# Kernel tuning notes

Measured on AMD Instinct MI355X. Metric: run time of the kernel, lower is better.

Reference implementation:

```python
import jax, jax.numpy as jnp
import numpy as np

N, D, H, E, K = 4096, 512, 2048, 8, 2  # tokens, input_size, hidden_size, num_experts, top_k


def setup_inputs() -> dict:
    key = jax.random.key(0)
    ks = jax.random.split(key, 4)
    x = jax.random.normal(ks[0], (N, D), dtype=jnp.float32)
    # torch init: weights ~ N(0, 0.001), biases zero
    Wg = jax.random.normal(ks[1], (D, E), dtype=jnp.float32) * 0.001
    bg = jnp.zeros((E,), jnp.float32)
    W1 = jax.random.normal(ks[2], (E, D, H), dtype=jnp.float32) * 0.001
    b1 = jnp.zeros((E, H), jnp.float32)
    W2 = jax.random.normal(ks[3], (E, H, D), dtype=jnp.float32) * 0.001
    b2 = jnp.zeros((E, D), jnp.float32)
    return {"x": x, "Wg": Wg, "bg": bg, "W1": W1, "b1": b1, "W2": W2, "b2": b2}


def reference(x, Wg, bg, W1, b1, W2, b2):
    # Gating: softmax over experts
    gates = jax.nn.softmax(x @ Wg + bg, axis=-1)            # [N, E]
    top_w, top_i = jax.lax.top_k(gates, K)                  # [N, K]
    top_w = top_w / jnp.sum(top_w, axis=-1, keepdims=True)  # renormalize

    # Expert MLP (fc1 -> fc2, no nonlinearity per source). Vectorized across all
    # experts, then gather the top-k selected outputs per token.
    h1 = jnp.einsum('nd,edh->neh', x, W1) + b1              # [N, E, H]
    all_out = jnp.einsum('neh,ehd->ned', h1, W2) + b2       # [N, E, D]
    sel = jnp.take_along_axis(all_out, top_i[:, :, None], axis=1)  # [N, K, D]

    combined = jnp.einsum('nkd,nk->nd', sel, top_w)         # [N, D]

    # usage counts: scatter-add of (detached) top-k weights per expert
    usage = jnp.zeros((E,), x.dtype).at[top_i.reshape(-1)].add(
        jax.lax.stop_gradient(top_w).reshape(-1))
    return combined, usage
```

## Files before the change

kernel.cpp:

```cpp
#include <hip/hip_runtime.h>
#include <hip/hip_bf16.h>


#define N_TOK 4096
#define DIM   512
#define HID   2048
#define NEXP  8
#define TOTSLOT (2 * N_TOK)
#define M1TILE 72
#define M2TILE 144

typedef __attribute__((ext_vector_type(8))) short short8;
typedef __attribute__((ext_vector_type(4))) float f32x4;

static __device__ __forceinline__ unsigned short f2bf(float f) {
    __hip_bfloat16 b = __float2bfloat16(f);
    return *reinterpret_cast<unsigned short*>(&b);
}
static __device__ __forceinline__ float bf2f(unsigned short u) {
    return __uint_as_float((unsigned)u << 16);
}

static __device__ __forceinline__ void load16_to_lds(const void* g, void* l) {
    __builtin_amdgcn_global_load_lds(
        (const __attribute__((address_space(1))) unsigned int*)g,
        (__attribute__((address_space(3))) unsigned int*)l, 16, 0, 0);
}

__global__ __launch_bounds__(256) void gating_kernel(
    const float* __restrict__ x, const float* __restrict__ Wg,
    const float* __restrict__ bg,
    int* __restrict__ cnt, int* __restrict__ te, float* __restrict__ tw,
    float* __restrict__ usage, unsigned short* __restrict__ Xb)
{
    __shared__ int   lcnt[NEXP];
    __shared__ float lus[NEXP];
    int tid = threadIdx.x;
    if (tid < NEXP) { lcnt[tid] = 0; lus[tid] = 0.f; }
    __syncthreads();

    int wave = tid >> 6;
    int lane = tid & 63;

    for (int t = 0; t < 4; ++t) {
        int n = blockIdx.x * 16 + wave * 4 + t;

        float acc[NEXP];
#pragma unroll
        for (int e = 0; e < NEXP; ++e) acc[e] = 0.f;

#pragma unroll
        for (int it = 0; it < DIM / 64; ++it) {
            int d = it * 64 + lane;
            float xv = x[n * DIM + d];
            Xb[n * DIM + d] = f2bf(xv);
            float4 wa = *(const float4*)&Wg[d * NEXP];
            float4 wb = *(const float4*)&Wg[d * NEXP + 4];
            acc[0] += xv * wa.x; acc[1] += xv * wa.y;
            acc[2] += xv * wa.z; acc[3] += xv * wa.w;
            acc[4] += xv * wb.x; acc[5] += xv * wb.y;
            acc[6] += xv * wb.z; acc[7] += xv * wb.w;
        }
#pragma unroll
        for (int m = 32; m >= 1; m >>= 1) {
#pragma unroll
            for (int e = 0; e < NEXP; ++e)
                acc[e] += __shfl_xor(acc[e], m, 64);
        }
        if (lane == 0) {
            float l[NEXP];
#pragma unroll
            for (int e = 0; e < NEXP; ++e) l[e] = acc[e] + bg[e];
            int i0 = 0;
#pragma unroll
            for (int e = 1; e < NEXP; ++e) if (l[e] > l[i0]) i0 = e;
            int i1 = (i0 == 0) ? 1 : 0;
#pragma unroll
            for (int e = 0; e < NEXP; ++e)
                if (e != i0 && l[e] > l[i1]) i1 = e;
            float w0 = 1.f / (1.f + expf(l[i1] - l[i0]));
            float w1 = 1.f - w0;
            te[n * 2] = i0; te[n * 2 + 1] = i1;
            tw[n * 2] = w0; tw[n * 2 + 1] = w1;
            atomicAdd(&lcnt[i0], 1);
            atomicAdd(&lcnt[i1], 1);
            atomicAdd(&lus[i0], w0);
            atomicAdd(&lus[i1], w1);
        }
    }
    __syncthreads();
    if (tid < NEXP) {
        if (lcnt[tid]) atomicAdd(&cnt[tid], lcnt[tid]);
        if (lus[tid] != 0.f) atomicAdd(&usage[tid], lus[tid]);
    }
}

__global__ void prefix_kernel(const int* __restrict__ cnt,
                              int* __restrict__ offs, int* __restrict__ fill,
                              int* __restrict__ tb128, int* __restrict__ tb64,
                              int* __restrict__ ntile)
{
    if (threadIdx.x == 0) {
        int s = 0, a = 0, b = 0;
        for (int e = 0; e < NEXP; ++e) {
            offs[e] = s; s += cnt[e];
            tb128[e] = a; a += (cnt[e] + 127) >> 7;
            tb64[e]  = b; b += (cnt[e] + 63) >> 6;
        }
        tb128[NEXP] = a; tb64[NEXP] = b;
        ntile[0] = a; ntile[1] = b;
    }
    if (threadIdx.x < NEXP) fill[threadIdx.x] = 0;
}

__global__ __launch_bounds__(256) void scatter_kernel(
    int* __restrict__ te, const float* __restrict__ tw,
    const int* __restrict__ offs, int* __restrict__ fill,
    int* __restrict__ btok, float* __restrict__ bwt)
{
    __shared__ int lcnt[NEXP];
    __shared__ int gbase[NEXP];
    int tid = threadIdx.x;
    if (tid < NEXP) lcnt[tid] = 0;
    __syncthreads();
    int n = blockIdx.x * 256 + tid;
    int e0 = te[n * 2], e1 = te[n * 2 + 1];
    int l0 = atomicAdd(&lcnt[e0], 1);
    int l1 = atomicAdd(&lcnt[e1], 1);
    __syncthreads();
    if (tid < NEXP) gbase[tid] = atomicAdd(&fill[tid], lcnt[tid]);
    __syncthreads();
    int s0 = offs[e0] + gbase[e0] + l0;
    int s1 = offs[e1] + gbase[e1] + l1;
    btok[s0] = n; bwt[s0] = tw[n * 2];
    btok[s1] = n; bwt[s1] = tw[n * 2 + 1];
    te[n * 2] = s0; te[n * 2 + 1] = s1;
}

__global__ __launch_bounds__(256) void transpose_cvt_kernel(
    const float* __restrict__ in, unsigned short* __restrict__ out,
    int R, int C)
{
    __shared__ unsigned short tile[64][65];
    int e = blockIdx.z;
    const float* src = in + (size_t)e * R * C;
    unsigned short* dst = out + (size_t)e * R * C;
    int r0 = blockIdx.x * 64, c0 = blockIdx.y * 64;
    int tid = threadIdx.x;
    int rr = tid >> 2, cb = (tid & 3) * 16;
#pragma unroll
    for (int i = 0; i < 4; ++i) {
        float4 v = *(const float4*)&src[(size_t)(r0 + rr) * C + c0 + cb + i * 4];
        tile[rr][cb + i * 4 + 0] = f2bf(v.x);
        tile[rr][cb + i * 4 + 1] = f2bf(v.y);
        tile[rr][cb + i * 4 + 2] = f2bf(v.z);
        tile[rr][cb + i * 4 + 3] = f2bf(v.w);
    }
    __syncthreads();
#pragma unroll
    for (int i = 0; i < 4; ++i) {
        ushort4 u;
        u.x = tile[cb + i * 4 + 0][rr];
        u.y = tile[cb + i * 4 + 1][rr];
        u.z = tile[cb + i * 4 + 2][rr];
        u.w = tile[cb + i * 4 + 3][rr];
        *(ushort4*)&dst[(size_t)(c0 + rr) * R + r0 + cb + i * 4] = u;
    }
}


__global__ __launch_bounds__(256) void gemm1_kernel(
    const unsigned short* __restrict__ Xb, const unsigned short* __restrict__ W1t,
    const float* __restrict__ b1, const int* __restrict__ cnt,
    const int* __restrict__ offs, const int* __restrict__ btok,
    const int* __restrict__ tb128, const int* __restrict__ ntile,
    unsigned short* __restrict__ H1)
{
    __shared__ __align__(16) unsigned short Ws[128 * 64];
    __shared__ __align__(16) unsigned short Xs[128 * 64];
    __shared__ int tok_s[128];

    int bx = blockIdx.x;
    int ti = (bx & 7) * (M1TILE / 8) + (bx >> 3);
    if (ti >= ntile[0]) return;
    int e = 0;
#pragma unroll
    for (int k = 1; k < NEXP; ++k) if (ti >= tb128[k]) e = k;
    int tt = ti - tb128[e];
    int ht = blockIdx.y;
    int cn = cnt[e];
    int off_e = offs[e];
    int tid = threadIdx.x;

    if (tid < 128) {
        int lr = tt * 128 + tid;
        tok_s[tid] = (lr < cn) ? btok[off_e + lr] : 0;
    }
    __syncthreads();

    int wave = tid >> 6, lane = tid & 63;
    int mbase = (wave >> 1) * 64, nbase = (wave & 1) * 64;
    int quad = lane >> 4, lcol = lane & 15;
    f32x4 acc[4][4];
#pragma unroll
    for (int mi = 0; mi < 4; ++mi)
#pragma unroll
        for (int ni = 0; ni < 4; ++ni)
            acc[mi][ni] = (f32x4){0.f, 0.f, 0.f, 0.f};

    int Rb = tid >> 3, pc = tid & 7;
    const unsigned short* Wsrc = W1t + ((size_t)e * HID + ht * 128) * DIM;

    for (int k0 = 0; k0 < DIM; k0 += 64) {
#pragma unroll
        for (int p = 0; p < 4; ++p) {
            int R = Rb + p * 32;
            int c = pc ^ (R & 7);
            load16_to_lds(&Wsrc[(size_t)R * DIM + k0 + c * 8], &Ws[R * 64 + pc * 8]);
            load16_to_lds(&Xb[(size_t)tok_s[R] * DIM + k0 + c * 8], &Xs[R * 64 + pc * 8]);
        }
        __syncthreads();
#pragma unroll
        for (int h = 0; h < 2; ++h) {
            int cs = ((h * 4 + quad) ^ (lcol & 7)) * 8;
            short8 a[4], b[4];
#pragma unroll
            for (int i = 0; i < 4; ++i) {
                a[i] = *(const short8*)&Ws[(mbase + i * 16 + lcol) * 64 + cs];
                b[i] = *(const short8*)&Xs[(nbase + i * 16 + lcol) * 64 + cs];
            }
#pragma unroll
            for (int mi = 0; mi < 4; ++mi)
#pragma unroll
                for (int ni = 0; ni < 4; ++ni)
                    acc[mi][ni] = __builtin_amdgcn_mfma_f32_16x16x32_bf16(
                        a[mi], b[ni], acc[mi][ni], 0, 0, 0);
        }
        __syncthreads();
    }

    float4 bv[4];
#pragma unroll
    for (int mi = 0; mi < 4; ++mi)
        bv[mi] = *(const float4*)&b1[e * HID + ht * 128 + mbase + mi * 16 + quad * 4];
#pragma unroll
    for (int ni = 0; ni < 4; ++ni) {
        int tn = tt * 128 + nbase + ni * 16 + lcol;
        if (tn >= cn) continue;
        size_t srow = (size_t)(off_e + tn) * HID + ht * 128;
#pragma unroll
        for (int mi = 0; mi < 4; ++mi) {
            int hh = mbase + mi * 16 + quad * 4;
            ushort4 u;
            u.x = f2bf(acc[mi][ni][0] + bv[mi].x);
            u.y = f2bf(acc[mi][ni][1] + bv[mi].y);
            u.z = f2bf(acc[mi][ni][2] + bv[mi].z);
            u.w = f2bf(acc[mi][ni][3] + bv[mi].w);
            *(ushort4*)&H1[srow + hh] = u;
        }
    }
}

#define KSPLIT 2
#define KCH (HID / KSPLIT)

__global__ __launch_bounds__(256) void gemm2_kernel(
    const unsigned short* __restrict__ H1, const unsigned short* __restrict__ W2t,
    const float* __restrict__ b2, const int* __restrict__ cnt,
    const int* __restrict__ offs, const float* __restrict__ bwt,
    const int* __restrict__ tb64, const int* __restrict__ ntile,
    unsigned short* __restrict__ O)
{
    __shared__ __align__(16) unsigned short Ws[128 * 64];
    __shared__ __align__(16) unsigned short Hs[64 * 64];
    __shared__ float wt_s[64];

    int bx = blockIdx.x;
    int ti = (bx & 7) * (M2TILE / 8) + (bx >> 3);
    if (ti >= ntile[1]) return;
    int e = 0;
#pragma unroll
    for (int k = 1; k < NEXP; ++k) if (ti >= tb64[k]) e = k;
    int tt = ti - tb64[e];
    int dt = blockIdx.y, kz = blockIdx.z;
    int cn = cnt[e];
    int off_e = offs[e];
    int sb = off_e + tt * 64;
    int tid = threadIdx.x;

    if (tid < 64) {
        int lr = tt * 64 + tid;
        wt_s[tid] = (lr < cn) ? bwt[off_e + lr] : 0.f;
    }

    int wave = tid >> 6, lane = tid & 63;
    int nbase = wave * 32;
    int quad = lane >> 4, lcol = lane & 15;
    f32x4 acc[4][2];
#pragma unroll
    for (int mi = 0; mi < 4; ++mi)
#pragma unroll
        for (int ni = 0; ni < 2; ++ni)
            acc[mi][ni] = (f32x4){0.f, 0.f, 0.f, 0.f};

    int Rb = tid >> 3, pc = tid & 7;
    const unsigned short* Wsrc = W2t + ((size_t)e * DIM + dt * 128) * HID;

    for (int k0 = kz * KCH; k0 < (kz + 1) * KCH; k0 += 64) {
#pragma unroll
        for (int p = 0; p < 4; ++p) {
            int R = Rb + p * 32;
            int c = pc ^ (R & 7);
            load16_to_lds(&Wsrc[(size_t)R * HID + k0 + c * 8], &Ws[R * 64 + pc * 8]);
        }
#pragma unroll
        for (int p = 0; p < 2; ++p) {
            int R = Rb + p * 32;
            int c = pc ^ (R & 7);
            int sr = sb + R; if (sr > TOTSLOT - 1) sr = TOTSLOT - 1;
            load16_to_lds(&H1[(size_t)sr * HID + k0 + c * 8], &Hs[R * 64 + pc * 8]);
        }
        __syncthreads();
#pragma unroll
        for (int h = 0; h < 2; ++h) {
            int cs = ((h * 4 + quad) ^ (lcol & 7)) * 8;
            short8 a[4], b[2];
#pragma unroll
            for (int i = 0; i < 4; ++i)
                a[i] = *(const short8*)&Hs[(i * 16 + lcol) * 64 + cs];
#pragma unroll
            for (int i = 0; i < 2; ++i)
                b[i] = *(const short8*)&Ws[(nbase + i * 16 + lcol) * 64 + cs];
#pragma unroll
            for (int mi = 0; mi < 4; ++mi)
#pragma unroll
                for (int ni = 0; ni < 2; ++ni)
                    acc[mi][ni] = __builtin_amdgcn_mfma_f32_16x16x32_bf16(
                        a[mi], b[ni], acc[mi][ni], 0, 0, 0);
        }
        __syncthreads();
    }

    unsigned short* Oe = O + ((size_t)kz * TOTSLOT + sb) * DIM + dt * 128;
#pragma unroll
    for (int ni = 0; ni < 2; ++ni) {
        int dl = nbase + ni * 16 + lcol;
        float bv = (kz == 0) ? b2[e * DIM + dt * 128 + dl] : 0.f;
#pragma unroll
        for (int mi = 0; mi < 4; ++mi) {
            int rl = mi * 16 + quad * 4;
#pragma unroll
            for (int r = 0; r < 4; ++r) {
                int sl = rl + r;
                if (tt * 64 + sl < cn)
                    Oe[(size_t)sl * DIM + dl] = f2bf(wt_s[sl] * (acc[mi][ni][r] + bv));
            }
        }
    }
}

__global__ __launch_bounds__(256) void combine_kernel(
    const unsigned short* __restrict__ O, const int* __restrict__ sidx,
    float* __restrict__ out)
{
    int tid = threadIdx.x;
    int n = blockIdx.x * 2 + (tid >> 7);
    int dd = (tid & 127) * 4;
    int s0 = sidx[n * 2], s1 = sidx[n * 2 + 1];
    ushort4 a = *(const ushort4*)&O[(size_t)s0 * DIM + dd];
    ushort4 b = *(const ushort4*)&O[((size_t)TOTSLOT + s0) * DIM + dd];
    ushort4 c = *(const ushort4*)&O[(size_t)s1 * DIM + dd];
    ushort4 d = *(const ushort4*)&O[((size_t)TOTSLOT + s1) * DIM + dd];
    float4 o;
    o.x = bf2f(a.x) + bf2f(b.x) + bf2f(c.x) + bf2f(d.x);
    o.y = bf2f(a.y) + bf2f(b.y) + bf2f(c.y) + bf2f(d.y);
    o.z = bf2f(a.z) + bf2f(b.z) + bf2f(c.z) + bf2f(d.z);
    o.w = bf2f(a.w) + bf2f(b.w) + bf2f(c.w) + bf2f(d.w);
    *(float4*)&out[(size_t)n * DIM + dd] = o;
}

#define TN 16
#define HC 256
#define NCHUNK (HID / HC)

__global__ __launch_bounds__(256) void gating_fb_kernel(
    const float* __restrict__ x, const float* __restrict__ Wg,
    const float* __restrict__ bg,
    int* __restrict__ cnt, int* __restrict__ btok, float* __restrict__ bwt,
    float* __restrict__ usage)
{
    int wave = threadIdx.x >> 6;
    int lane = threadIdx.x & 63;
    int n = blockIdx.x * 4 + wave;
    float acc[NEXP];
#pragma unroll
    for (int e = 0; e < NEXP; ++e) acc[e] = 0.f;
    for (int d = lane; d < DIM; d += 64) {
        float xv = x[n * DIM + d];
        float4 wa = *(const float4*)&Wg[d * NEXP];
        float4 wb = *(const float4*)&Wg[d * NEXP + 4];
        acc[0] += xv * wa.x; acc[1] += xv * wa.y;
        acc[2] += xv * wa.z; acc[3] += xv * wa.w;
        acc[4] += xv * wb.x; acc[5] += xv * wb.y;
        acc[6] += xv * wb.z; acc[7] += xv * wb.w;
    }
#pragma unroll
    for (int m = 32; m >= 1; m >>= 1)
#pragma unroll
        for (int e = 0; e < NEXP; ++e)
            acc[e] += __shfl_xor(acc[e], m, 64);
    if (lane == 0) {
        float l[NEXP];
#pragma unroll
        for (int e = 0; e < NEXP; ++e) l[e] = acc[e] + bg[e];
        int i0 = 0;
#pragma unroll
        for (int e = 1; e < NEXP; ++e) if (l[e] > l[i0]) i0 = e;
        int i1 = (i0 == 0) ? 1 : 0;
#pragma unroll
        for (int e = 0; e < NEXP; ++e)
            if (e != i0 && l[e] > l[i1]) i1 = e;
        float w0 = 1.f / (1.f + expf(l[i1] - l[i0]));
        float w1 = 1.f - w0;
        int p0 = atomicAdd(&cnt[i0], 1);
        btok[i0 * N_TOK + p0] = n; bwt[i0 * N_TOK + p0] = w0;
        int p1 = atomicAdd(&cnt[i1], 1);
        btok[i1 * N_TOK + p1] = n; bwt[i1 * N_TOK + p1] = w1;
        atomicAdd(&usage[i0], w0);
        atomicAdd(&usage[i1], w1);
    }
}

__global__ __launch_bounds__(256) void expert_fb_kernel(
    const float* __restrict__ x, const float* __restrict__ W1,
    const float* __restrict__ b1, const float* __restrict__ W2,
    const float* __restrict__ b2, const int* __restrict__ cnt,
    const int* __restrict__ btok, const float* __restrict__ bwt,
    float* __restrict__ out)
{
    __shared__ float xs[TN][DIM];
    __shared__ float h1s[TN][HC];
    __shared__ int   tok_s[TN];
    __shared__ float wt_s[TN];
    int e = blockIdx.x >> 8;
    int tile = blockIdx.x & 255;
    int cn = cnt[e];
    int n0 = tile * TN;
    if (n0 >= cn) return;
    int nt = min(TN, cn - n0);
    int tid = threadIdx.x;
    if (tid < TN) {
        if (tid < nt) { tok_s[tid] = btok[e * N_TOK + n0 + tid]; wt_s[tid] = bwt[e * N_TOK + n0 + tid]; }
        else          { tok_s[tid] = 0; wt_s[tid] = 0.f; }
    }
    __syncthreads();
    for (int idx = tid; idx < TN * DIM; idx += 256) {
        int t = idx >> 9, d = idx & 511;
        xs[t][d] = (t < nt) ? x[tok_s[t] * DIM + d] : 0.f;
    }
    const float* W1e = W1 + (size_t)e * DIM * HID;
    const float* W2e = W2 + (size_t)e * HID * DIM;
    int tg = tid >> 6, lane = tid & 63;
    float oacc[4][8];
    {
        float4 ba = *(const float4*)&b2[e * DIM + lane * 8];
        float4 bb = *(const float4*)&b2[e * DIM + lane * 8 + 4];
#pragma unroll
        for (int ti = 0; ti < 4; ++ti) {
            oacc[ti][0] = ba.x; oacc[ti][1] = ba.y; oacc[ti][2] = ba.z; oacc[ti][3] = ba.w;
            oacc[ti][4] = bb.x; oacc[ti][5] = bb.y; oacc[ti][6] = bb.z; oacc[ti][7] = bb.w;
        }
    }
    __syncthreads();
    for (int ch = 0; ch < NCHUNK; ++ch) {
        int h0 = ch * HC;
        float f[4][4];
        {
            float4 b1v = *(const float4*)&b1[e * HID + h0 + lane * 4];
#pragma unroll
            for (int ti = 0; ti < 4; ++ti) {
                f[ti][0] = b1v.x; f[ti][1] = b1v.y; f[ti][2] = b1v.z; f[ti][3] = b1v.w;
            }
        }
        for (int d = 0; d < DIM; ++d) {
            float4 w1v = *(const float4*)&W1e[(size_t)d * HID + h0 + lane * 4];
#pragma unroll
            for (int ti = 0; ti < 4; ++ti) {
                float xv = xs[tg + 4 * ti][d];
                f[ti][0] += xv * w1v.x; f[ti][1] += xv * w1v.y;
                f[ti][2] += xv * w1v.z; f[ti][3] += xv * w1v.w;
            }
        }
        __syncthreads();
#pragma unroll
        for (int ti = 0; ti < 4; ++ti)
            *(float4*)&h1s[tg + 4 * ti][lane * 4] = make_float4(f[ti][0], f[ti][1], f[ti][2], f[ti][3]);
        __syncthreads();
        for (int j = 0; j < HC; ++j) {
            const float* w2row = &W2e[(size_t)(h0 + j) * DIM + lane * 8];
            float4 wa = *(const float4*)w2row;
            float4 wb = *(const float4*)(w2row + 4);
#pragma unroll
            for (int ti = 0; ti < 4; ++ti) {
                float hv = h1s[tg + 4 * ti][j];
                oacc[ti][0] += hv * wa.x; oacc[ti][1] += hv * wa.y;
                oacc[ti][2] += hv * wa.z; oacc[ti][3] += hv * wa.w;
                oacc[ti][4] += hv * wb.x; oacc[ti][5] += hv * wb.y;
                oacc[ti][6] += hv * wb.z; oacc[ti][7] += hv * wb.w;
            }
        }
    }
#pragma unroll
    for (int ti = 0; ti < 4; ++ti) {
        int t = tg + 4 * ti;
        if (t < nt) {
            float w = wt_s[t];
            float* o = &out[(size_t)tok_s[t] * DIM + lane * 8];
#pragma unroll
            for (int c = 0; c < 8; ++c)
                atomicAdd(&o[c], w * oacc[ti][c]);
        }
    }
}

extern "C" void kernel_launch(void* const* d_in, const int* in_sizes, int n_in,
                              void* d_out, int out_size, void* d_ws, size_t ws_size,
                              hipStream_t stream) {
    const float* x  = (const float*)d_in[0];
    const float* Wg = (const float*)d_in[1];
    const float* bg = (const float*)d_in[2];
    const float* W1 = (const float*)d_in[3];
    const float* b1 = (const float*)d_in[4];
    const float* W2 = (const float*)d_in[5];
    const float* b2 = (const float*)d_in[6];

    float* out   = (float*)d_out;
    float* usage = out + (size_t)N_TOK * DIM;

    char* ws = (char*)d_ws;
    int*   cnt   = (int*)(ws + 0);
    int*   fill  = (int*)(ws + 32);
    int*   offs  = (int*)(ws + 64);
    int*   tb128 = (int*)(ws + 96);
    int*   tb64  = (int*)(ws + 132);
    int*   ntile = (int*)(ws + 168);
    int*   te   = (int*)(ws + 256);
    float* tw   = (float*)(ws + 33024);
    int*   btok = (int*)(ws + 65792);
    float* bwt  = (float*)(ws + 98560);
    unsigned short* Xb  = (unsigned short*)(ws + 131328);
    unsigned short* W1t = (unsigned short*)(ws + 4325632);
    unsigned short* O   = W1t;
    unsigned short* W2t = (unsigned short*)(ws + 21102848);
    unsigned short* H1  = (unsigned short*)(ws + 37880064);
    const size_t WS_NEED = 71434496ULL;

    if (ws_size >= WS_NEED) {
        hipMemsetAsync(cnt, 0, 32, stream);
        hipMemsetAsync(usage, 0, NEXP * sizeof(float), stream);
        transpose_cvt_kernel<<<dim3(DIM / 64, HID / 64, NEXP), 256, 0, stream>>>(W1, W1t, DIM, HID);
        transpose_cvt_kernel<<<dim3(HID / 64, DIM / 64, NEXP), 256, 0, stream>>>(W2, W2t, HID, DIM);
        gating_kernel<<<N_TOK / 16, 256, 0, stream>>>(x, Wg, bg, cnt, te, tw, usage, Xb);
        prefix_kernel<<<1, 64, 0, stream>>>(cnt, offs, fill, tb128, tb64, ntile);
        scatter_kernel<<<N_TOK / 256, 256, 0, stream>>>(te, tw, offs, fill, btok, bwt);
        gemm1_kernel<<<dim3(M1TILE, HID / 128), 256, 0, stream>>>(
            Xb, W1t, b1, cnt, offs, btok, tb128, ntile, H1);
        gemm2_kernel<<<dim3(M2TILE, DIM / 128, KSPLIT), 256, 0, stream>>>(
            H1, W2t, b2, cnt, offs, bwt, tb64, ntile, O);
        combine_kernel<<<N_TOK / 2, 256, 0, stream>>>(O, te, out);
    } else {
        int*   fcnt  = (int*)d_ws;
        int*   fbtok = (int*)((char*)d_ws + 256);
        float* fbwt  = (float*)((char*)d_ws + 256 + (size_t)NEXP * N_TOK * sizeof(int));
        hipMemsetAsync(d_out, 0, (size_t)(N_TOK * DIM + NEXP) * sizeof(float), stream);
        hipMemsetAsync(d_ws, 0, 256, stream);
        gating_fb_kernel<<<N_TOK / 4, 256, 0, stream>>>(x, Wg, bg, fcnt, fbtok, fbwt, usage);
        expert_fb_kernel<<<NEXP * (N_TOK / TN), 256, 0, stream>>>(
            x, W1, b1, W2, b2, fcnt, fbtok, fbwt, out);
    }
}
```

Baseline: 212.0 us.

## Double-buffer LDS tiles in both expert GEMMs to overlap loads with MFMA

Both grouped GEMM kernels now keep two LDS buffers per operand. Each iteration issues the global-to-LDS loads for the next K tile before computing on the current one, and waits with partial vmcnt counts. This is meant to hide global memory latency behind the MFMA work. In exchange, LDS use per block doubles, which may lower occupancy, and correctness depends on the hand-written vmcnt values matching the number of loads issued per stage.

After: 217.1 us. +2.4%, slower.

```diff
diff --git a/kernel.cpp b/kernel.cpp
--- a/kernel.cpp
+++ b/kernel.cpp
@@ -176,8 +176,8 @@
     const int* __restrict__ tb128, const int* __restrict__ ntile,
     unsigned short* __restrict__ H1)
 {
-    __shared__ __align__(16) unsigned short Ws[128 * 64];
-    __shared__ __align__(16) unsigned short Xs[128 * 64];
+    __shared__ __align__(16) unsigned short Ws[2][128 * 64];
+    __shared__ __align__(16) unsigned short Xs[2][128 * 64];
     __shared__ int tok_s[128];
 
     int bx = blockIdx.x;
@@ -211,23 +211,37 @@
     int Rb = tid >> 3, pc = tid & 7;
     const unsigned short* Wsrc = W1t + ((size_t)e * HID + ht * 128) * DIM;
 
-    for (int k0 = 0; k0 < DIM; k0 += 64) {
+    auto stage = [&](int buf, int k0) {
 #pragma unroll
         for (int p = 0; p < 4; ++p) {
             int R = Rb + p * 32;
             int c = pc ^ (R & 7);
-            load16_to_lds(&Wsrc[(size_t)R * DIM + k0 + c * 8], &Ws[R * 64 + pc * 8]);
-            load16_to_lds(&Xb[(size_t)tok_s[R] * DIM + k0 + c * 8], &Xs[R * 64 + pc * 8]);
-        }
-        __syncthreads();
+            load16_to_lds(&Wsrc[(size_t)R * DIM + k0 + c * 8], &Ws[buf][R * 64 + pc * 8]);
+            load16_to_lds(&Xb[(size_t)tok_s[R] * DIM + k0 + c * 8], &Xs[buf][R * 64 + pc * 8]);
+        }
+    };
+
+    stage(0, 0);
+
+    const int NT = DIM / 64;
+    for (int t = 0; t < NT; ++t) {
+        int cur = t & 1;
+        if (t + 1 < NT) {
+            stage(cur ^ 1, (t + 1) * 64);
+            asm volatile("s_waitcnt vmcnt(8)" ::: "memory");
+        } else {
+            asm volatile("s_waitcnt vmcnt(0)" ::: "memory");
+        }
+        __builtin_amdgcn_s_barrier();
+        __builtin_amdgcn_sched_barrier(0);
 #pragma unroll
         for (int h = 0; h < 2; ++h) {
             int cs = ((h * 4 + quad) ^ (lcol & 7)) * 8;
             short8 a[4], b[4];
 #pragma unroll
             for (int i = 0; i < 4; ++i) {
-                a[i] = *(const short8*)&Ws[(mbase + i * 16 + lcol) * 64 + cs];
-                b[i] = *(const short8*)&Xs[(nbase + i * 16 + lcol) * 64 + cs];
+                a[i] = *(const short8*)&Ws[cur][(mbase + i * 16 + lcol) * 64 + cs];
+                b[i] = *(const short8*)&Xs[cur][(nbase + i * 16 + lcol) * 64 + cs];
             }
 #pragma unroll
             for (int mi = 0; mi < 4; ++mi)
@@ -236,7 +250,8 @@
                     acc[mi][ni] = __builtin_amdgcn_mfma_f32_16x16x32_bf16(
                         a[mi], b[ni], acc[mi][ni], 0, 0, 0);
         }
-        __syncthreads();
+        __builtin_amdgcn_sched_barrier(0);
+        __builtin_amdgcn_s_barrier();
     }
 
     float4 bv[4];
@@ -271,8 +286,8 @@
     const int* __restrict__ tb64, const int* __restrict__ ntile,
     unsigned short* __restrict__ O)
 {
-    __shared__ __align__(16) unsigned short Ws[128 * 64];
-    __shared__ __align__(16) unsigned short Hs[64 * 64];
+    __shared__ __align__(16) unsigned short Ws[2][128 * 64];
+    __shared__ __align__(16) unsigned short Hs[2][64 * 64];
     __shared__ float wt_s[64];
 
     int bx = blockIdx.x;
@@ -306,31 +321,45 @@
     int Rb = tid >> 3, pc = tid & 7;
     const unsigned short* Wsrc = W2t + ((size_t)e * DIM + dt * 128) * HID;
 
-    for (int k0 = kz * KCH; k0 < (kz + 1) * KCH; k0 += 64) {
+    auto stage = [&](int buf, int k0) {
 #pragma unroll
         for (int p = 0; p < 4; ++p) {
             int R = Rb + p * 32;
             int c = pc ^ (R & 7);
-            load16_to_lds(&Wsrc[(size_t)R * HID + k0 + c * 8], &Ws[R * 64 + pc * 8]);
+            load16_to_lds(&Wsrc[(size_t)R * HID + k0 + c * 8], &Ws[buf][R * 64 + pc * 8]);
         }
 #pragma unroll
         for (int p = 0; p < 2; ++p) {
             int R = Rb + p * 32;
             int c = pc ^ (R & 7);
             int sr = sb + R; if (sr > TOTSLOT - 1) sr = TOTSLOT - 1;
-            load16_to_lds(&H1[(size_t)sr * HID + k0 + c * 8], &Hs[R * 64 + pc * 8]);
-        }
-        __syncthreads();
+            load16_to_lds(&H1[(size_t)sr * HID + k0 + c * 8], &Hs[buf][R * 64 + pc * 8]);
+        }
+    };
+
+    stage(0, kz * KCH);
+
+    const int NT = KCH / 64;
+    for (int t = 0; t < NT; ++t) {
+        int cur = t & 1;
+        if (t + 1 < NT) {
+            stage(cur ^ 1, kz * KCH + (t + 1) * 64);
+            asm volatile("s_waitcnt vmcnt(6)" ::: "memory");
+        } else {
+            asm volatile("s_waitcnt vmcnt(0)" ::: "memory");
+        }
+        __builtin_amdgcn_s_barrier();
+        __builtin_amdgcn_sched_barrier(0);
 #pragma unroll
         for (int h = 0; h < 2; ++h) {
             int cs = ((h * 4 + quad) ^ (lcol & 7)) * 8;
             short8 a[4], b[2];
 #pragma unroll
             for (int i = 0; i < 4; ++i)
-                a[i] = *(const short8*)&Hs[(i * 16 + lcol) * 64 + cs];
+                a[i] = *(const short8*)&Hs[cur][(i * 16 + lcol) * 64 + cs];
 #pragma unroll
             for (int i = 0; i < 2; ++i)
-                b[i] = *(const short8*)&Ws[(nbase + i * 16 + lcol) * 64 + cs];
+                b[i] = *(const short8*)&Ws[cur][(nbase + i * 16 + lcol) * 64 + cs];
 #pragma unroll
             for (int mi = 0; mi < 4; ++mi)
 #pragma unroll
@@ -338,7 +367,8 @@
                     acc[mi][ni] = __builtin_amdgcn_mfma_f32_16x16x32_bf16(
                         a[mi], b[ni], acc[mi][ni], 0, 0, 0);
         }
-        __syncthreads();
+        __builtin_amdgcn_sched_barrier(0);
+        __builtin_amdgcn_s_barrier();
     }
 
     unsigned short* Oe = O + ((size_t)kz * TOTSLOT + sb) * DIM + dt * 128;
```
